# Kernel tuning notes

Hardware: AMD Instinct MI355X
Metric: run time of the kernel (lower is better)

## Reference

```python
import jax, jax.numpy as jnp
import numpy as np

D_MODEL = 1024
NUM_HEAD = 16
CHUNK = 64
NGROUPS = 2
D_HEAD = D_MODEL // NUM_HEAD
NEG = -1e30


def setup_inputs() -> dict:
    key = jax.random.key(0)
    ks = jax.random.split(key, 4)
    bs, seq = 2, 4096
    proj_dim = 3 * D_MODEL + 2 * NGROUPS * D_HEAD
    hidden = jax.random.normal(ks[0], (bs, seq, D_MODEL), jnp.float32)
    W_in = jax.random.normal(ks[1], (D_MODEL, proj_dim), jnp.float32) * (D_MODEL ** -0.5)
    # torch init: uniform_(1, chunk_size-1) then log
    gate_bias = jnp.log(jax.random.uniform(ks[2], (D_MODEL,), jnp.float32, 1.0, CHUNK - 1.0))
    rms_weight = jnp.ones((D_MODEL,), jnp.float32)
    W_out = jax.random.normal(ks[3], (D_MODEL, D_MODEL), jnp.float32) * (D_MODEL ** -0.5)
    return {"hidden_states": hidden, "rms_weight": rms_weight, "W_in": W_in,
            "gate_bias": gate_bias, "W_out": W_out}


def _scan_op(a, b):
    ga, xa = a
    gb, xb = b
    return gb * ga, gb * xa + xb


def reference(hidden_states, rms_weight, W_in, gate_bias, W_out):
    bs, seq, d = hidden_states.shape
    dh = d // NUM_HEAD
    nc = seq // CHUNK
    scale = dh ** -0.5
    rep = NUM_HEAD // NGROUPS

    shortcut = hidden_states
    # RMSNorm
    h = hidden_states * jax.lax.rsqrt(jnp.mean(hidden_states ** 2, axis=-1, keepdims=True) + 1e-6) * rms_weight
    proj = h @ W_in  # [bs, seq, 3d + 2*ng*dh]
    z, x, g, q, k = jnp.split(proj, [d, 2 * d, 3 * d, 3 * d + NGROUPS * dh], axis=-1)
    z = jax.nn.sigmoid(z)
    g = jax.nn.sigmoid(g + gate_bias)

    # repeat grouped q/k across heads (torch .repeat tiles)
    q = jnp.tile(q, (1, 1, rep))
    k = jnp.tile(k, (1, 1, rep))
    qh = q.reshape(bs, seq, NUM_HEAD, dh).transpose(0, 2, 1, 3)  # [b,h,s,dh]

    xc = x.reshape(bs, nc, CHUNK, d)
    gc = g.reshape(bs, nc, CHUNK, d)
    kc = k.reshape(bs, nc, CHUNK, d)
    g2 = jnp.concatenate([gc, gc], axis=-1)           # g.repeat(1,1,1,2)
    v = (1.0 - g2) * jnp.concatenate([xc, kc], axis=-1)
    # gated linear recurrence within each chunk: y_t = g_t*y_{t-1} + v_t
    _, xk = jax.lax.associative_scan(_scan_op, (g2, v), axis=2)

    intra_x = xk[..., :d].reshape(bs, seq, NUM_HEAD, dh).transpose(0, 2, 1, 3)  # [b,h,s,dh]
    intra_k = xk[..., d:].reshape(bs, seq, NUM_HEAD, dh).transpose(0, 2, 1, 3)

    # one kv per chunk (position 0 of each chunk, per torch [..., ::chunk_size, :])
    chunk_k = intra_k[:, :, ::CHUNK, :]  # [b,h,nc,dh]
    chunk_x = intra_x[:, :, ::CHUNK, :]

    # inter-chunk block-causal attention: query in chunk c attends kv chunks < c
    scores = jnp.einsum('bhsd,bhcd->bhsc', qh, chunk_k) * scale
    allowed = (jnp.arange(seq)[:, None] // CHUNK) > jnp.arange(nc)[None, :]  # [s,nc]
    masked = jnp.where(allowed, scores, NEG)

    # intra lse: per-token self dot product
    intra_lse = jnp.einsum('bhsd,bhsd->bhs', qh, intra_k) * scale

    # fused, numerically-stable version of flex_attention + MergeLastToken
    m = jnp.maximum(jnp.max(masked, axis=-1), intra_lse)  # [b,h,s], finite
    w = jnp.exp(masked - m[..., None])                     # zeros where masked
    intra_w = jnp.exp(intra_lse - m)
    denom = jnp.sum(w, axis=-1) + intra_w
    out = (jnp.einsum('bhsc,bhcd->bhsd', w, chunk_x) + intra_w[..., None] * intra_x) / denom[..., None]

    out = out.transpose(0, 2, 1, 3).reshape(bs, seq, d)
    return (z * out) @ W_out + shortcut
```

## Files before the change

kernel.cpp:

```cpp
#include <hip/hip_runtime.h>
#include <hip/hip_bf16.h>

typedef __bf16 bf16x8 __attribute__((ext_vector_type(8)));
typedef __bf16 bf16x4 __attribute__((ext_vector_type(4)));
typedef float  f32x4  __attribute__((ext_vector_type(4)));

#define DM 1024
#define PD 3328
#define TROWS 8192
#define SEQ 4096

__device__ __forceinline__ float sigmoidf(float x) { return 1.f / (1.f + __expf(-x)); }

__device__ __forceinline__ void gload16(const void* g, void* l) {
  __builtin_amdgcn_global_load_lds(
      (const __attribute__((address_space(1))) void*)g,
      (__attribute__((address_space(3))) void*)l, 16, 0, 0);
}

__global__ __launch_bounds__(256) void prep_kernel(const float* __restrict__ Win,
                                                   __bf16* __restrict__ WinT,
                                                   const float* __restrict__ Wout,
                                                   __bf16* __restrict__ WoutT,
                                                   const float* __restrict__ hidden,
                                                   const float* __restrict__ rmsw,
                                                   __bf16* __restrict__ hbf) {
  const int id = blockIdx.x;
  const int tid = threadIdx.x;
  if (id < 4352) {
    __shared__ float tile[32][33];
    const float* in;  __bf16* out;  int K, N, bx, by;
    if (id < 3328) { in = Win;  out = WinT;  K = DM; N = PD; bx = id % 104; by = id / 104; }
    else           { in = Wout; out = WoutT; K = DM; N = DM; bx = (id - 3328) & 31; by = (id - 3328) >> 5; }
    int n0 = bx * 32, k0 = by * 32;
    int tx = tid & 31, ty = tid >> 5;
    for (int i = ty; i < 32; i += 8) tile[i][tx] = in[(size_t)(k0 + i) * N + n0 + tx];
    __syncthreads();
    for (int i = ty; i < 32; i += 8) out[(size_t)(n0 + i) * K + k0 + tx] = (__bf16)tile[tx][i];
  } else {
    int r = id - 4352;
    float4 v = ((const float4*)(hidden + (size_t)r * DM))[tid];
    float ss = v.x * v.x + v.y * v.y + v.z * v.z + v.w * v.w;
#pragma unroll
    for (int off = 32; off > 0; off >>= 1) ss += __shfl_xor(ss, off);
    __shared__ float wsum[4];
    int lane = tid & 63, wid = tid >> 6;
    if (lane == 0) wsum[wid] = ss;
    __syncthreads();
    float tot = wsum[0] + wsum[1] + wsum[2] + wsum[3];
    float inv = rsqrtf(tot * (1.f / 1024.f) + 1e-6f);
    float4 wl = ((const float4*)rmsw)[tid];
    bf16x4 o;
    o[0] = (__bf16)(v.x * inv * wl.x);
    o[1] = (__bf16)(v.y * inv * wl.y);
    o[2] = (__bf16)(v.z * inv * wl.z);
    o[3] = (__bf16)(v.w * inv * wl.w);
    *(bf16x4*)(hbf + (size_t)r * DM + tid * 4) = o;
  }
}

template <int GM, int GN, int EPI>
__global__ __launch_bounds__(512, 4) void gemm21(
    const __bf16* __restrict__ A, const __bf16* __restrict__ Bt,
    int N_out, int K,
    const float* __restrict__ gate_bias, const float* __restrict__ shortcut,
    float* __restrict__ outf, __bf16* __restrict__ zbf, __bf16* __restrict__ xbf,
    __bf16* __restrict__ gbf, __bf16* __restrict__ qbf, __bf16* __restrict__ kbf) {
  __shared__ __bf16 As[2][256 * 32];
  __shared__ __bf16 Bs[2][128 * 32];

  const int tid = threadIdx.x;
  const int lane = tid & 63, wid = tid >> 6;
  const int wm = wid >> 1, wn = wid & 1;
  const int lr = lane & 15, hh = lane >> 4;

  const int nwg = gridDim.x, cpx = nwg >> 3;
  const int swz = (blockIdx.x & 7) * cpx + (blockIdx.x >> 3);
  const int ntx = N_out >> 7;
  const int ngn = ntx / GN;
  const int g = swz / (GM * GN), l = swz % (GM * GN);
  const int gm = g / ngn, gn = g % ngn;
  const int m0 = (gm * GM + (l % GM)) << 8;
  const int n0 = (gn * GN + (l / GM)) << 7;

  f32x4 acc[4][4] = {};
  const int NT = K >> 5;

  const int arow0 = wm * 64 + lr;
  const int brow0 = wn * 64 + lr;

  auto stageA = [&](int kt, __bf16* lbuf) {
#pragma unroll
    for (int j = 0; j < 2; ++j) {
      int c = tid + j * 512;
      int row = c >> 2, s = c & 3;
      int lsw = s ^ ((row >> 1) & 3);
      gload16(&A[(size_t)(m0 + row) * K + kt + lsw * 8], lbuf + c * 8);
    }
  };
  auto stageB = [&](int kt, __bf16* lbuf) {
    int c = tid;
    int row = c >> 2, s = c & 3;
    int lsw = s ^ ((row >> 1) & 3);
    gload16(&Bt[(size_t)(n0 + row) * K + kt + lsw * 8], lbuf + c * 8);
  };
  auto fragrd = [&](const __bf16* buf, int row) -> bf16x8 {
    int s = hh ^ ((row >> 1) & 3);
    return *(const bf16x8*)&buf[(row << 5) + (s << 3)];
  };

  stageA(0, &As[0][0]);
  stageB(0, &Bs[0][0]);
  asm volatile("s_waitcnt vmcnt(0)" ::: "memory");
  __builtin_amdgcn_s_barrier();

  for (int t = 0; t < NT; ++t) {
    const __bf16* Ap = &As[t & 1][0];
    const __bf16* Bp = &Bs[t & 1][0];
    if (t + 1 < NT) {
      stageA((t + 1) << 5, &As[(t + 1) & 1][0]);
      stageB((t + 1) << 5, &Bs[(t + 1) & 1][0]);
    }
    {
      bf16x8 af[4], bf[4];
#pragma unroll
      for (int m = 0; m < 4; ++m) af[m] = fragrd(Ap, arow0 + m * 16);
#pragma unroll
      for (int n = 0; n < 4; ++n) bf[n] = fragrd(Bp, brow0 + n * 16);
      __builtin_amdgcn_s_setprio(1);
#pragma unroll
      for (int m = 0; m < 4; ++m)
#pragma unroll
        for (int n = 0; n < 4; ++n)
          acc[m][n] = __builtin_amdgcn_mfma_f32_16x16x32_bf16(af[m], bf[n], acc[m][n], 0, 0, 0);
      __builtin_amdgcn_s_setprio(0);
    }
    asm volatile("s_waitcnt vmcnt(0)" ::: "memory");
    __builtin_amdgcn_s_barrier();
  }

#pragma unroll
  for (int m = 0; m < 4; ++m) {
#pragma unroll
    for (int n = 0; n < 4; ++n) {
#pragma unroll
      for (int i = 0; i < 4; ++i) {
        int r = m0 + wm * 64 + m * 16 + (hh << 2) + i;
        int c = n0 + wn * 64 + n * 16 + lr;
        float v = acc[m][n][i];
        if (EPI == 1) {
          if (c < 1024)       zbf[(size_t)r * DM + c] = (__bf16)sigmoidf(v);
          else if (c < 2048)  xbf[(size_t)r * DM + (c - 1024)] = (__bf16)v;
          else if (c < 3072)  gbf[(size_t)r * DM + (c - 2048)] = (__bf16)sigmoidf(v + gate_bias[c - 2048]);
          else if (c < 3200)  qbf[(size_t)r * 128 + (c - 3072)] = (__bf16)v;
          else                kbf[(size_t)r * 128 + (c - 3200)] = (__bf16)v;
        } else {
          outf[(size_t)r * DM + c] = v + shortcut[(size_t)r * DM + c];
        }
      }
    }
  }
}

template <int GN, int EPI>
__global__ __launch_bounds__(512, 4) void gemm2p(
    const __bf16* __restrict__ A, const __bf16* __restrict__ Bt,
    int N_out, int K,
    const float* __restrict__ gate_bias, const float* __restrict__ shortcut,
    float* __restrict__ outf, __bf16* __restrict__ zbf, __bf16* __restrict__ xbf,
    __bf16* __restrict__ gbf, __bf16* __restrict__ qbf, __bf16* __restrict__ kbf) {
  __shared__ __bf16 As[2][128 * 64];
  __shared__ __bf16 Bs[2][128 * 64];

  const int tid = threadIdx.x;
  const int lane = tid & 63, wid = tid >> 6;
  const int wr = wid >> 1, wc = wid & 1;

  const int nwg = gridDim.x;
  const int cpx = nwg >> 3;
  const int swz = (blockIdx.x & 7) * cpx + (blockIdx.x >> 3);
  const int ntx = N_out >> 7;
  const int ngn = ntx / GN;
  const int g = swz / (8 * GN), l = swz % (8 * GN);
  const int gm = g / ngn, gn = g % ngn;
  const int m0 = (gm * 8 + (l & 7)) << 7;
  const int n0 = (gn * GN + (l >> 3)) << 7;

  f32x4 acc[2][4] = {};
  const int NT = K >> 6;

  const int arow0 = wr * 32 + (lane & 15);
  const int brow0 = wc * 64 + (lane & 15);

  auto stage = [&](const __bf16* src, int row0, int kt, __bf16* lbuf) {
#pragma unroll
    for (int j = 0; j < 2; ++j) {
      int off16 = tid + j * 512;
      int row = off16 >> 3, slot = off16 & 7;
      int col = (slot ^ (row & 7)) << 3;
      gload16(&src[(size_t)(row0 + row) * K + kt + col], lbuf + off16 * 8);
    }
  };
  auto fragrd = [&](const __bf16* buf, int row, int ks) -> bf16x8 {
    int s = ((ks << 2) + (lane >> 4)) ^ (row & 7);
    return *(const bf16x8*)&buf[(row << 6) + (s << 3)];
  };

  stage(A, m0, 0, &As[0][0]);
  stage(Bt, n0, 0, &Bs[0][0]);
  asm volatile("s_waitcnt vmcnt(0)" ::: "memory");
  __builtin_amdgcn_s_barrier();

  for (int t = 0; t < NT; ++t) {
    const __bf16* Ap = &As[t & 1][0];
    const __bf16* Bp = &Bs[t & 1][0];
    if (t + 1 < NT) {
      stage(A, m0, (t + 1) << 6, &As[(t + 1) & 1][0]);
      stage(Bt, n0, (t + 1) << 6, &Bs[(t + 1) & 1][0]);
    }
#pragma unroll
    for (int ks = 0; ks < 2; ++ks) {
      bf16x8 af[2], bf[4];
#pragma unroll
      for (int m = 0; m < 2; ++m) af[m] = fragrd(Ap, arow0 + m * 16, ks);
#pragma unroll
      for (int n = 0; n < 4; ++n) bf[n] = fragrd(Bp, brow0 + n * 16, ks);
      __builtin_amdgcn_s_setprio(1);
#pragma unroll
      for (int m = 0; m < 2; ++m)
#pragma unroll
        for (int n = 0; n < 4; ++n)
          acc[m][n] = __builtin_amdgcn_mfma_f32_16x16x32_bf16(af[m], bf[n], acc[m][n], 0, 0, 0);
      __builtin_amdgcn_s_setprio(0);
    }
    asm volatile("s_waitcnt vmcnt(0)" ::: "memory");
    __builtin_amdgcn_s_barrier();
  }

#pragma unroll
  for (int m = 0; m < 2; ++m) {
#pragma unroll
    for (int n = 0; n < 4; ++n) {
#pragma unroll
      for (int i = 0; i < 4; ++i) {
        int r = m0 + wr * 32 + m * 16 + ((lane >> 4) << 2) + i;
        int c = n0 + wc * 64 + n * 16 + (lane & 15);
        float v = acc[m][n][i];
        if (EPI == 1) {
          if (c < 1024)       zbf[(size_t)r * DM + c] = (__bf16)sigmoidf(v);
          else if (c < 2048)  xbf[(size_t)r * DM + (c - 1024)] = (__bf16)v;
          else if (c < 3072)  gbf[(size_t)r * DM + (c - 2048)] = (__bf16)sigmoidf(v + gate_bias[c - 2048]);
          else if (c < 3200)  qbf[(size_t)r * 128 + (c - 3072)] = (__bf16)v;
          else                kbf[(size_t)r * 128 + (c - 3200)] = (__bf16)v;
        } else {
          outf[(size_t)r * DM + c] = v + shortcut[(size_t)r * DM + c];
        }
      }
    }
  }
}

__global__ __launch_bounds__(256) void scan_kernel(const __bf16* __restrict__ g,
                                                   const __bf16* __restrict__ x,
                                                   const __bf16* __restrict__ kin,
                                                   __bf16* __restrict__ ixa,
                                                   __bf16* __restrict__ ika,
                                                   __bf16* __restrict__ cxtg) {
  int bx = blockIdx.x;
  int part = bx & 3;
  int c = (bx >> 2) & 63;
  int b = bx >> 8;
  int d = part * 256 + threadIdx.x;
  size_t base = (size_t)b * SEQ + (size_t)c * 64;
  float sx = 0.f, sk = 0.f;
  for (int t = 0; t < 64; ++t) {
    size_t row = base + t;
    float gg = (float)g[row * DM + d];
    float xv = (float)x[row * DM + d];
    float kv = (float)kin[row * 128 + (d & 127)];
    sx = gg * (sx - xv) + xv;
    sk = gg * (sk - kv) + kv;
    ixa[row * DM + d] = (__bf16)sx;
    ika[row * DM + d] = (__bf16)sk;
    if (t == 0) cxtg[((size_t)b * DM + d) * 64 + c] = (__bf16)sx;
  }
}

__global__ __launch_bounds__(256) void attn_kernel(const __bf16* __restrict__ qbf,
                                                   const __bf16* __restrict__ ixa,
                                                   const __bf16* __restrict__ ika,
                                                   const __bf16* __restrict__ cxtg,
                                                   const __bf16* __restrict__ zbf,
                                                   __bf16* __restrict__ y) {
  const int qt = blockIdx.x;
  const int h  = blockIdx.y;
  const int b  = blockIdx.z;
  const int tid = threadIdx.x;
  const int lane = tid & 63, wd = tid >> 6;

  __shared__ __bf16 qs[64 * 72];
  __shared__ __bf16 ck[64 * 72];
  __shared__ __bf16 cxT[64 * 72];
  __shared__ __bf16 pb[64 * 72];
  __shared__ float sc[64 * 65];
  __shared__ float rden[64], iwd[64], rlse[64];

  const size_t base = (size_t)b * SEQ;

  for (int i = tid; i < 512; i += 256) {
    int row = i >> 3, part = i & 7;
    *(bf16x8*)&qs[row * 72 + part * 8] =
        *(const bf16x8*)&qbf[(base + qt * 64 + row) * 128 + (h & 1) * 64 + part * 8];
    *(bf16x8*)&ck[row * 72 + part * 8] =
        *(const bf16x8*)&ika[(base + (size_t)row * 64) * DM + h * 64 + part * 8];
    *(bf16x8*)&cxT[row * 72 + part * 8] =
        *(const bf16x8*)&cxtg[((size_t)b * DM + h * 64 + row) * 64 + part * 8];
  }
  __syncthreads();

  {
    f32x4 d4[4] = {};
#pragma unroll
    for (int kk = 0; kk < 64; kk += 32) {
      bf16x8 a = *(const bf16x8*)&qs[(wd * 16 + (lane & 15)) * 72 + kk + (lane >> 4) * 8];
#pragma unroll
      for (int ni = 0; ni < 4; ++ni) {
        bf16x8 bb = *(const bf16x8*)&ck[(ni * 16 + (lane & 15)) * 72 + kk + (lane >> 4) * 8];
        d4[ni] = __builtin_amdgcn_mfma_f32_16x16x32_bf16(a, bb, d4[ni], 0, 0, 0);
      }
    }
#pragma unroll
    for (int ni = 0; ni < 4; ++ni)
#pragma unroll
      for (int i = 0; i < 4; ++i) {
        int qrow = wd * 16 + (lane >> 4) * 4 + i;
        int c = ni * 16 + (lane & 15);
        sc[qrow * 65 + c] = 0.125f * d4[ni][i];
      }
  }

  {
    int s = tid >> 2, p = tid & 3;
    const __bf16* krow = &ika[(base + qt * 64 + s) * DM + h * 64 + p * 16];
    float dot = 0.f;
#pragma unroll
    for (int half = 0; half < 2; ++half) {
      bf16x8 qa = *(const bf16x8*)&qs[s * 72 + p * 16 + half * 8];
      bf16x8 ka = *(const bf16x8*)&krow[half * 8];
#pragma unroll
      for (int e = 0; e < 8; ++e) dot += (float)qa[e] * (float)ka[e];
    }
    dot += __shfl_xor(dot, 1);
    dot += __shfl_xor(dot, 2);
    if (p == 0) rlse[s] = 0.125f * dot;
  }
  __syncthreads();

  {
    int s = tid >> 2, p = tid & 3;
    float lse = rlse[s];
    float m = -1e30f;
#pragma unroll
    for (int k = 0; k < 16; ++k) {
      int c = p * 16 + k;
      if (c < qt) m = fmaxf(m, sc[s * 65 + c]);
    }
    m = fmaxf(m, __shfl_xor(m, 1));
    m = fmaxf(m, __shfl_xor(m, 2));
    m = fmaxf(m, lse);
    float den = 0.f;
    bf16x8 w0, w1;
#pragma unroll
    for (int k = 0; k < 16; ++k) {
      int c = p * 16 + k;
      float wv = (c < qt) ? __expf(sc[s * 65 + c] - m) : 0.f;
      if (k < 8) w0[k] = (__bf16)wv; else w1[k - 8] = (__bf16)wv;
      den += wv;
    }
    *(bf16x8*)&pb[s * 72 + p * 16] = w0;
    *(bf16x8*)&pb[s * 72 + p * 16 + 8] = w1;
    den += __shfl_xor(den, 1);
    den += __shfl_xor(den, 2);
    float iw = __expf(lse - m);
    if (p == 0) {
      rden[s] = 1.f / (den + iw);
      iwd[s] = iw;
    }
  }
  __syncthreads();

  {
    f32x4 d4[4] = {};
#pragma unroll
    for (int kk = 0; kk < 64; kk += 32) {
      bf16x8 a = *(const bf16x8*)&pb[(wd * 16 + (lane & 15)) * 72 + kk + (lane >> 4) * 8];
#pragma unroll
      for (int ni = 0; ni < 4; ++ni) {
        bf16x8 bb = *(const bf16x8*)&cxT[(ni * 16 + (lane & 15)) * 72 + kk + (lane >> 4) * 8];
        d4[ni] = __builtin_amdgcn_mfma_f32_16x16x32_bf16(a, bb, d4[ni], 0, 0, 0);
      }
    }
#pragma unroll
    for (int ni = 0; ni < 4; ++ni)
#pragma unroll
      for (int i = 0; i < 4; ++i) {
        int qrow = wd * 16 + (lane >> 4) * 4 + i;
        int j = ni * 16 + (lane & 15);
        size_t srow = base + qt * 64 + qrow;
        float ix = (float)ixa[srow * DM + h * 64 + j];
        float outv = (d4[ni][i] + iwd[qrow] * ix) * rden[qrow];
        float zv = (float)zbf[srow * DM + h * 64 + j];
        y[srow * DM + h * 64 + j] = (__bf16)(outv * zv);
      }
  }
}

extern "C" void kernel_launch(void* const* d_in, const int* in_sizes, int n_in,
                              void* d_out, int out_size, void* d_ws, size_t ws_size,
                              hipStream_t stream) {
  const float* hidden = (const float*)d_in[0];
  const float* rmsw   = (const float*)d_in[1];
  const float* Win    = (const float*)d_in[2];
  const float* gbias  = (const float*)d_in[3];
  const float* Wout   = (const float*)d_in[4];
  float* out = (float*)d_out;

  char* ws = (char*)d_ws;
  size_t o = 0;
  auto alloc = [&](size_t bytes) { char* p = ws + o; o += (bytes + 255) & ~(size_t)255; return p; };
  __bf16* WinT  = (__bf16*)alloc((size_t)PD * DM * 2);
  __bf16* WoutT = (__bf16*)alloc((size_t)DM * DM * 2);
  __bf16* hy    = (__bf16*)alloc((size_t)TROWS * DM * 2);
  __bf16* zbf   = (__bf16*)alloc((size_t)TROWS * DM * 2);
  __bf16* xbf   = (__bf16*)alloc((size_t)TROWS * DM * 2);
  __bf16* gbf   = (__bf16*)alloc((size_t)TROWS * DM * 2);
  __bf16* qbf   = (__bf16*)alloc((size_t)TROWS * 128 * 2);
  __bf16* kbf   = (__bf16*)alloc((size_t)TROWS * 128 * 2);
  __bf16* ixa   = (__bf16*)alloc((size_t)TROWS * DM * 2);
  __bf16* ika   = (__bf16*)alloc((size_t)TROWS * DM * 2);
  __bf16* cxtg  = (__bf16*)alloc((size_t)2 * DM * 64 * 2);

  prep_kernel<<<dim3(12544), 256, 0, stream>>>(Win, WinT, Wout, WoutT, hidden, rmsw, hy);
  gemm21<4, 13, 1><<<dim3(832), 512, 0, stream>>>(
      hy, WinT, PD, DM, gbias, nullptr, nullptr, zbf, xbf, gbf, qbf, kbf);
  scan_kernel<<<512, 256, 0, stream>>>(gbf, xbf, kbf, ixa, ika, cxtg);
  attn_kernel<<<dim3(64, 16, 2), 256, 0, stream>>>(qbf, ixa, ika, cxtg, zbf, hy);
  gemm2p<8, 0><<<dim3((TROWS / 128) * (DM / 128)), 512, 0, stream>>>(
      hy, WoutT, DM, DM, nullptr, hidden, out, nullptr, nullptr, nullptr, nullptr, nullptr);
}
```

Before: 166.4 us.

## Replace input-projection GEMM with 256x256 tile, 8-wave ping-pong pipelined kernel

Swaps the 256x128-tile input projection GEMM for a 256x256-tile kernel with 8 waves arranged 2x4. The K step grows to 64 and is split into two halves, with global-to-LDS loads for the next steps interleaved between the four MFMA phases and separated by barriers. This is meant to improve operand reuse per LDS byte and to overlap memory traffic with compute. It uses more LDS and accumulator registers (occupancy of 2 blocks per CU) and runs half as many workgroups, with 416 blocks over the CUs, which risks tail imbalance.

Result: slower. 186.4 us (+12.0%).

```diff
diff --git a/kernel.cpp b/kernel.cpp
--- a/kernel.cpp
+++ b/kernel.cpp
@@ -16,6 +16,12 @@
   __builtin_amdgcn_global_load_lds(
       (const __attribute__((address_space(1))) void*)g,
       (__attribute__((address_space(3))) void*)l, 16, 0, 0);
+}
+
+__device__ __forceinline__ void barx() {
+  asm volatile("" ::: "memory");
+  __builtin_amdgcn_s_barrier();
+  asm volatile("" ::: "memory");
 }
 
 __global__ __launch_bounds__(256) void prep_kernel(const float* __restrict__ Win,
@@ -59,95 +65,142 @@
   }
 }
 
-template <int GM, int GN, int EPI>
-__global__ __launch_bounds__(512, 4) void gemm21(
+template <int EPI>
+__global__ __launch_bounds__(512, 2) void gemm8p(
     const __bf16* __restrict__ A, const __bf16* __restrict__ Bt,
     int N_out, int K,
     const float* __restrict__ gate_bias, const float* __restrict__ shortcut,
     float* __restrict__ outf, __bf16* __restrict__ zbf, __bf16* __restrict__ xbf,
     __bf16* __restrict__ gbf, __bf16* __restrict__ qbf, __bf16* __restrict__ kbf) {
-  __shared__ __bf16 As[2][256 * 32];
-  __shared__ __bf16 Bs[2][128 * 32];
+  __shared__ __bf16 Ah[2][2][256 * 32];
+  __shared__ __bf16 Bh[2][2][256 * 32];
 
   const int tid = threadIdx.x;
   const int lane = tid & 63, wid = tid >> 6;
-  const int wm = wid >> 1, wn = wid & 1;
+  const int wm = wid >> 2, wn = wid & 3;
   const int lr = lane & 15, hh = lane >> 4;
 
   const int nwg = gridDim.x, cpx = nwg >> 3;
   const int swz = (blockIdx.x & 7) * cpx + (blockIdx.x >> 3);
-  const int ntx = N_out >> 7;
-  const int ngn = ntx / GN;
-  const int g = swz / (GM * GN), l = swz % (GM * GN);
-  const int gm = g / ngn, gn = g % ngn;
-  const int m0 = (gm * GM + (l % GM)) << 8;
-  const int n0 = (gn * GN + (l / GM)) << 7;
-
-  f32x4 acc[4][4] = {};
-  const int NT = K >> 5;
-
-  const int arow0 = wm * 64 + lr;
-  const int brow0 = wn * 64 + lr;
-
-  auto stageA = [&](int kt, __bf16* lbuf) {
+  const int ntx = N_out >> 8;
+  const int m0 = (swz / ntx) << 8, n0 = (swz % ntx) << 8;
+
+  f32x4 acc[8][4] = {};
+  const int NT = K >> 6;
+
+  auto stA = [&](int t, int kh) {
+    __bf16* dst = &Ah[t & 1][kh][0];
+    const int kc = (t << 6) + (kh << 5);
 #pragma unroll
     for (int j = 0; j < 2; ++j) {
       int c = tid + j * 512;
       int row = c >> 2, s = c & 3;
-      int lsw = s ^ ((row >> 1) & 3);
-      gload16(&A[(size_t)(m0 + row) * K + kt + lsw * 8], lbuf + c * 8);
+      int ls = s ^ ((row >> 1) & 3);
+      gload16(&A[(size_t)(m0 + row) * K + kc + ls * 8], dst + c * 8);
     }
   };
-  auto stageB = [&](int kt, __bf16* lbuf) {
-    int c = tid;
-    int row = c >> 2, s = c & 3;
-    int lsw = s ^ ((row >> 1) & 3);
-    gload16(&Bt[(size_t)(n0 + row) * K + kt + lsw * 8], lbuf + c * 8);
+  auto stB = [&](int t, int kh) {
+    __bf16* dst = &Bh[t & 1][kh][0];
+    const int kc = (t << 6) + (kh << 5);
+#pragma unroll
+    for (int j = 0; j < 2; ++j) {
+      int c = tid + j * 512;
+      int row = c >> 2, s = c & 3;
+      int ls = s ^ ((row >> 1) & 3);
+      gload16(&Bt[(size_t)(n0 + row) * K + kc + ls * 8], dst + c * 8);
+    }
   };
-  auto fragrd = [&](const __bf16* buf, int row) -> bf16x8 {
+  auto frg = [&](const __bf16* hp, int row) -> bf16x8 {
     int s = hh ^ ((row >> 1) & 3);
-    return *(const bf16x8*)&buf[(row << 5) + (s << 3)];
+    return *(const bf16x8*)&hp[(row << 5) + (s << 3)];
   };
 
-  stageA(0, &As[0][0]);
-  stageB(0, &Bs[0][0]);
-  asm volatile("s_waitcnt vmcnt(0)" ::: "memory");
-  __builtin_amdgcn_s_barrier();
+  const int ar = wm * 128 + lr;
+  const int br = wn * 64 + lr;
+
+  stA(0, 0); stB(0, 0); stA(0, 1); stB(0, 1); stA(1, 0); stB(1, 0);
+  asm volatile("s_waitcnt vmcnt(4)" ::: "memory");
+  barx();
 
   for (int t = 0; t < NT; ++t) {
-    const __bf16* Ap = &As[t & 1][0];
-    const __bf16* Bp = &Bs[t & 1][0];
-    if (t + 1 < NT) {
-      stageA((t + 1) << 5, &As[(t + 1) & 1][0]);
-      stageB((t + 1) << 5, &Bs[(t + 1) & 1][0]);
-    }
-    {
-      bf16x8 af[4], bf[4];
-#pragma unroll
-      for (int m = 0; m < 4; ++m) af[m] = fragrd(Ap, arow0 + m * 16);
-#pragma unroll
-      for (int n = 0; n < 4; ++n) bf[n] = fragrd(Bp, brow0 + n * 16);
-      __builtin_amdgcn_s_setprio(1);
-#pragma unroll
-      for (int m = 0; m < 4; ++m)
-#pragma unroll
-        for (int n = 0; n < 4; ++n)
-          acc[m][n] = __builtin_amdgcn_mfma_f32_16x16x32_bf16(af[m], bf[n], acc[m][n], 0, 0, 0);
-      __builtin_amdgcn_s_setprio(0);
-    }
-    asm volatile("s_waitcnt vmcnt(0)" ::: "memory");
-    __builtin_amdgcn_s_barrier();
-  }
-
-#pragma unroll
-  for (int m = 0; m < 4; ++m) {
-#pragma unroll
-    for (int n = 0; n < 4; ++n) {
+    const __bf16* A0 = &Ah[t & 1][0][0];
+    const __bf16* A1 = &Ah[t & 1][1][0];
+    const __bf16* B0 = &Bh[t & 1][0][0];
+    const __bf16* B1 = &Bh[t & 1][1][0];
+    bf16x8 af[4], bfr[4];
+
+#pragma unroll
+    for (int mf = 0; mf < 4; ++mf) af[mf] = frg(A0, ar + mf * 16);
+#pragma unroll
+    for (int nf = 0; nf < 4; ++nf) bfr[nf] = frg(B0, br + nf * 16);
+    if (t + 1 < NT) stA(t + 1, 1);
+    barx();
+    asm volatile("s_waitcnt lgkmcnt(0)" ::: "memory");
+    __builtin_amdgcn_s_setprio(1);
+#pragma unroll
+    for (int mf = 0; mf < 4; ++mf)
+#pragma unroll
+      for (int nf = 0; nf < 4; ++nf)
+        acc[mf][nf] = __builtin_amdgcn_mfma_f32_16x16x32_bf16(af[mf], bfr[nf], acc[mf][nf], 0, 0, 0);
+    __builtin_amdgcn_s_setprio(0);
+    barx();
+
+#pragma unroll
+    for (int mf = 0; mf < 4; ++mf) af[mf] = frg(A0, ar + 64 + mf * 16);
+    if (t + 1 < NT) stB(t + 1, 1);
+    barx();
+    asm volatile("s_waitcnt lgkmcnt(0)" ::: "memory");
+    __builtin_amdgcn_s_setprio(1);
+#pragma unroll
+    for (int mf = 0; mf < 4; ++mf)
+#pragma unroll
+      for (int nf = 0; nf < 4; ++nf)
+        acc[4 + mf][nf] = __builtin_amdgcn_mfma_f32_16x16x32_bf16(af[mf], bfr[nf], acc[4 + mf][nf], 0, 0, 0);
+    __builtin_amdgcn_s_setprio(0);
+    barx();
+
+#pragma unroll
+    for (int mf = 0; mf < 4; ++mf) af[mf] = frg(A1, ar + mf * 16);
+#pragma unroll
+    for (int nf = 0; nf < 4; ++nf) bfr[nf] = frg(B1, br + nf * 16);
+    if (t + 2 < NT) stA(t + 2, 0);
+    barx();
+    asm volatile("s_waitcnt lgkmcnt(0)" ::: "memory");
+    __builtin_amdgcn_s_setprio(1);
+#pragma unroll
+    for (int mf = 0; mf < 4; ++mf)
+#pragma unroll
+      for (int nf = 0; nf < 4; ++nf)
+        acc[mf][nf] = __builtin_amdgcn_mfma_f32_16x16x32_bf16(af[mf], bfr[nf], acc[mf][nf], 0, 0, 0);
+    __builtin_amdgcn_s_setprio(0);
+    barx();
+
+#pragma unroll
+    for (int mf = 0; mf < 4; ++mf) af[mf] = frg(A1, ar + 64 + mf * 16);
+    if (t + 2 < NT) stB(t + 2, 0);
+    if (t + 2 < NT)      asm volatile("s_waitcnt vmcnt(4)" ::: "memory");
+    else if (t + 1 < NT) asm volatile("s_waitcnt vmcnt(0)" ::: "memory");
+    barx();
+    asm volatile("s_waitcnt lgkmcnt(0)" ::: "memory");
+    __builtin_amdgcn_s_setprio(1);
+#pragma unroll
+    for (int mf = 0; mf < 4; ++mf)
+#pragma unroll
+      for (int nf = 0; nf < 4; ++nf)
+        acc[4 + mf][nf] = __builtin_amdgcn_mfma_f32_16x16x32_bf16(af[mf], bfr[nf], acc[4 + mf][nf], 0, 0, 0);
+    __builtin_amdgcn_s_setprio(0);
+    barx();
+  }
+
+#pragma unroll
+  for (int mf = 0; mf < 8; ++mf) {
+#pragma unroll
+    for (int nf = 0; nf < 4; ++nf) {
 #pragma unroll
       for (int i = 0; i < 4; ++i) {
-        int r = m0 + wm * 64 + m * 16 + (hh << 2) + i;
-        int c = n0 + wn * 64 + n * 16 + lr;
-        float v = acc[m][n][i];
+        int r = m0 + wm * 128 + mf * 16 + (hh << 2) + i;
+        int c = n0 + wn * 64 + nf * 16 + lr;
+        float v = acc[mf][nf][i];
         if (EPI == 1) {
           if (c < 1024)       zbf[(size_t)r * DM + c] = (__bf16)sigmoidf(v);
           else if (c < 2048)  xbf[(size_t)r * DM + (c - 1024)] = (__bf16)v;
@@ -441,7 +494,7 @@
   __bf16* cxtg  = (__bf16*)alloc((size_t)2 * DM * 64 * 2);
 
   prep_kernel<<<dim3(12544), 256, 0, stream>>>(Win, WinT, Wout, WoutT, hidden, rmsw, hy);
-  gemm21<4, 13, 1><<<dim3(832), 512, 0, stream>>>(
+  gemm8p<1><<<dim3(416), 512, 0, stream>>>(
       hy, WinT, PD, DM, gbias, nullptr, nullptr, zbf, xbf, gbf, qbf, kbf);
   scan_kernel<<<512, 256, 0, stream>>>(gbf, xbf, kbf, ixa, ika, cxtg);
   attn_kernel<<<dim3(64, 16, 2), 256, 0, stream>>>(qbf, ixa, ika, cxtg, zbf, hy);
```
